# Kernel tuning notes

Hardware: AMD Instinct MI355X
Metric: run time of the kernel (lower is better)

Reference implementation:

```python
import jax, jax.numpy as jnp
import numpy as np

EPS = 1e-5  # torch LayerNorm default
NUM_HEADS = 8


def layernorm(x, g, b):
    m = jnp.mean(x, axis=-1, keepdims=True)
    v = jnp.var(x, axis=-1, keepdims=True)
    return (x - m) * jax.lax.rsqrt(v + EPS) * g + b


def dwconv(x_img, w, b):
    # x_img: [B,C,H,W]; w: [C,1,k,k] depthwise, 'same' padding
    C = x_img.shape[1]
    k = w.shape[-1]
    out = jax.lax.conv_general_dilated(
        x_img, w, (1, 1), [(k // 2, k // 2)] * 2,
        dimension_numbers=('NCHW', 'OIHW', 'NCHW'), feature_group_count=C)
    return out + b[None, :, None, None]


def _forward(x, domain_label, cpe_w, cpe_b, ln1_g, ln1_b, qkv_w, proj_w, proj_b,
             dl_w1, dl_b1, dl_w2, dl_b2, crpe_w3, crpe_b3, crpe_w5, crpe_b5,
             crpe_w7, crpe_b7, ln2_g, ln2_b, fc1_w, fc1_b, fc2_w, fc2_b, H, W, d):
    B, N, C = x.shape
    h = NUM_HEADS
    Ch = C // h
    scale = Ch ** (-0.5)

    # ---- CPE: depthwise 3x3 conv positional encoding with residual ----
    xi = x.transpose(0, 2, 1).reshape(B, C, H, W)
    xi = dwconv(xi, cpe_w, cpe_b) + xi
    x = xi.reshape(B, C, N).transpose(0, 2, 1)

    # ---- domain-indexed LayerNorm 1 (d is a static python int) ----
    cur = layernorm(x, ln1_g[d], ln1_b[d])

    # ---- factorized attention ----
    qkv = (cur @ qkv_w).reshape(B, N, 3, h, Ch).transpose(2, 0, 3, 1, 4)
    q, k, v = qkv[0], qkv[1], qkv[2]          # each [B,h,N,Ch]
    k_sm = jax.nn.softmax(k, axis=2)          # softmax over tokens
    kv = jnp.einsum('bhnk,bhnv->bhkv', k_sm, v)       # [B,h,Ch,Ch]
    factor_att = jnp.einsum('bhnk,bhkv->bhnv', q, kv)  # [B,h,N,Ch]

    # ---- conv relative position encoding (window splits {3:2,5:3,7:3}) ----
    v_img = v.transpose(0, 1, 3, 2).reshape(B, C, H, W)
    g1 = dwconv(v_img[:, :2 * Ch], crpe_w3, crpe_b3)
    g2 = dwconv(v_img[:, 2 * Ch:5 * Ch], crpe_w5, crpe_b5)
    g3 = dwconv(v_img[:, 5 * Ch:], crpe_w7, crpe_b7)
    conv_v = jnp.concatenate([g1, g2, g3], axis=1)        # [B,C,H,W]
    conv_v = conv_v.reshape(B, h, Ch, N).transpose(0, 1, 3, 2)
    crpe = q * conv_v                                      # [B,h,N,Ch]

    factor_att = scale * factor_att + crpe

    # ---- per-domain softmax gating over heads ----
    da = jax.nn.relu(domain_label @ dl_w1 + dl_b1) @ dl_w2 + dl_b2  # [B, h*Ch]
    da = da.reshape(B, h, Ch)[:, :, None, :]                        # [B,h,1,Ch]
    da = jax.nn.softmax(da, axis=1)                                  # over heads
    attn = (da * factor_att).transpose(0, 2, 1, 3).reshape(B, N, C)
    attn = attn @ proj_w + proj_b

    x = x + attn

    # ---- domain-indexed LayerNorm 2 + MLP ----
    cur = layernorm(x, ln2_g[d], ln2_b[d])
    cur = jax.nn.gelu(cur @ fc1_w + fc1_b, approximate=False) @ fc2_w + fc2_b
    return x + cur


def setup_inputs() -> dict:
    key = jax.random.key(0)
    ks = iter(jax.random.split(key, 32))
    B, H, W, C, h, nd = 8, 56, 56, 256, 8, 4
    N = H * W
    Ch = C // h
    hid = C // 2   # domain MLP hidden = max(dim//r,4), r=2
    mh = 4 * C     # mlp_ratio=4
    r = lambda shape, s=0.02: jax.random.normal(next(ks), shape, jnp.float32) * s
    return dict(
        x=jax.random.normal(next(ks), (B, N, C), jnp.float32),
        domain_label=jax.nn.one_hot(
            jax.random.randint(next(ks), (B,), 0, nd), nd, dtype=jnp.float32),
        cpe_w=r((C, 1, 3, 3)), cpe_b=jnp.zeros((C,), jnp.float32),
        ln1_g=jnp.ones((nd, C), jnp.float32), ln1_b=jnp.zeros((nd, C), jnp.float32),
        qkv_w=r((C, 3 * C)),
        proj_w=r((C, C)), proj_b=jnp.zeros((C,), jnp.float32),
        dl_w1=r((nd, hid)), dl_b1=jnp.zeros((hid,), jnp.float32),
        dl_w2=r((hid, C)), dl_b2=jnp.zeros((C,), jnp.float32),
        crpe_w3=r((2 * Ch, 1, 3, 3)), crpe_b3=jnp.zeros((2 * Ch,), jnp.float32),
        crpe_w5=r((3 * Ch, 1, 5, 5)), crpe_b5=jnp.zeros((3 * Ch,), jnp.float32),
        crpe_w7=r((3 * Ch, 1, 7, 7)), crpe_b7=jnp.zeros((3 * Ch,), jnp.float32),
        ln2_g=jnp.ones((nd, C), jnp.float32), ln2_b=jnp.zeros((nd, C), jnp.float32),
        fc1_w=r((C, mh)), fc1_b=jnp.zeros((mh,), jnp.float32),
        fc2_w=r((mh, C)), fc2_b=jnp.zeros((C,), jnp.float32),
        H=H, W=W, d=0,
    )


def reference(x, domain_label, cpe_w, cpe_b, ln1_g, ln1_b, qkv_w, proj_w, proj_b,
              dl_w1, dl_b1, dl_w2, dl_b2, crpe_w3, crpe_b3, crpe_w5, crpe_b5,
              crpe_w7, crpe_b7, ln2_g, ln2_b, fc1_w, fc1_b, fc2_w, fc2_b, H, W, d):
    return _forward(x, domain_label, cpe_w, cpe_b, ln1_g, ln1_b, qkv_w, proj_w,
                    proj_b, dl_w1, dl_b1, dl_w2, dl_b2, crpe_w3, crpe_b3, crpe_w5,
                    crpe_b5, crpe_w7, crpe_b7, ln2_g, ln2_b, fc1_w, fc1_b, fc2_w,
                    fc2_b, H, W, d)
```

## Files before the change

### kernel.cpp

```cpp
#include <hip/hip_runtime.h>
#include <hip/hip_bf16.h>
#include <math.h>

#define BB 8
#define HH 56
#define WW 56
#define NN (HH*WW)
#define CC 256
#define NH 8
#define NT (BB*NN)
#define HID 128
#define MH 1024
#define SCALE 0.17677669529663687f

typedef __attribute__((ext_vector_type(8))) short bf16x8;
typedef __attribute__((ext_vector_type(4))) float f32x4;

__device__ __forceinline__ ushort f2bf(float f) {
    __hip_bfloat16 h = __float2bfloat16(f);
    return *(ushort*)&h;
}
__device__ __forceinline__ uint pk2(float lo, float hi) {
    return ((uint)f2bf(hi) << 16) | (uint)f2bf(lo);
}
__device__ __forceinline__ float unlo(uint u) { return __uint_as_float(u << 16); }
__device__ __forceinline__ float unhi(uint u) { return __uint_as_float(u & 0xFFFF0000u); }

__device__ __forceinline__ void gload16(const void* g, void* s) {
    __builtin_amdgcn_global_load_lds(
        (const __attribute__((address_space(1))) void*)g,
        (__attribute__((address_space(3))) void*)s, 16, 0, 0);
}

__global__ __launch_bounds__(256) void wtrans_kernel(
    const float* __restrict__ w, ushort* __restrict__ wt, int K, int N)
{
    __shared__ float tile[32][33];
    const int t = threadIdx.x;
    const int col = t & 31, rw = t >> 5;
    const int k0 = blockIdx.y * 32, n0 = blockIdx.x * 32;
    #pragma unroll
    for (int i = rw; i < 32; i += 8)
        tile[i][col] = w[(size_t)(k0 + i) * N + n0 + col];
    __syncthreads();
    #pragma unroll
    for (int i = rw; i < 32; i += 8)
        wt[(size_t)(n0 + i) * K + k0 + col] = f2bf(tile[col][i]);
}

__global__ __launch_bounds__(256) void wpack_kernel(
    const float* __restrict__ w3, const float* __restrict__ b3,
    const float* __restrict__ w5, const float* __restrict__ b5,
    const float* __restrict__ w7, const float* __restrict__ b7,
    uint* __restrict__ wt, float* __restrict__ bt)
{
    const int qq = blockIdx.x;
    const int KSQ = (qq == 0) ? 3 : (qq == 1) ? 5 : 7;
    for (int idx = threadIdx.x; idx < 49 * 32; idx += 256) {
        int tap = idx >> 5, p = idx & 31;
        int cA = qq * 64 + 2 * p;
        float lo = 0.f, hi = 0.f;
        if (tap < KSQ * KSQ) {
            int dy = tap / KSQ, dx = tap - dy * KSQ;
            const float* wb; int kslo;
            if (cA < 64)       { wb = w3 + cA * 9;          kslo = 3; }
            else if (cA < 160) { wb = w5 + (cA - 64) * 25;  kslo = 5; }
            else               { wb = w7 + (cA - 160) * 49; kslo = 7; }
            int offp = KSQ / 2 - kslo / 2;
            int sy = dy - offp, sx = dx - offp;
            if (sy >= 0 && sy < kslo && sx >= 0 && sx < kslo) {
                lo = wb[sy * kslo + sx];
                hi = wb[kslo * kslo + sy * kslo + sx];
            }
        }
        wt[(qq * 49 + tap) * 32 + p] = pk2(lo, hi);
    }
    if (threadIdx.x < 32) {
        int p = threadIdx.x, cA = qq * 64 + 2 * p;
        float blo, bhi;
        if (cA < 64)       { blo = b3[cA];       bhi = b3[cA + 1]; }
        else if (cA < 160) { blo = b5[cA - 64];  bhi = b5[cA - 63]; }
        else               { blo = b7[cA - 160]; bhi = b7[cA - 159]; }
        bt[(qq * 32 + p) * 2]     = blo;
        bt[(qq * 32 + p) * 2 + 1] = bhi;
    }
}

__global__ __launch_bounds__(256) void cpack_kernel(
    const float* __restrict__ w, const float* __restrict__ bias,
    uint* __restrict__ wt, float* __restrict__ bt)
{
    const int qq = blockIdx.x;
    for (int idx = threadIdx.x; idx < 9 * 32; idx += 256) {
        int tap = idx >> 5, p = idx & 31;
        int cA = qq * 64 + 2 * p;
        wt[(qq * 9 + tap) * 32 + p] = pk2(w[cA * 9 + tap], w[(cA + 1) * 9 + tap]);
    }
    if (threadIdx.x < 32) {
        int p = threadIdx.x, cA = qq * 64 + 2 * p;
        bt[(qq * 32 + p) * 2]     = bias[cA];
        bt[(qq * 32 + p) * 2 + 1] = bias[cA + 1];
    }
}

__global__ __launch_bounds__(256) void cpe_kernel(
    const float* __restrict__ x, const uint* __restrict__ wtab,
    const float* __restrict__ btab, float* __restrict__ out)
{
    __shared__ uint vt[4 * 34 * 32];
    const int qq = blockIdx.x >> 1, hx = blockIdx.x & 1;
    const int y0 = blockIdx.y * 2, b = blockIdx.z;
    const int x0 = hx * 28;
    const int t = threadIdx.x;
    const int c0 = qq * 64;
    const int p = t & 31;

    uint wpk[9];
    #pragma unroll
    for (int i = 0; i < 9; ++i) wpk[i] = wtab[(qq * 9 + i) * 32 + p];
    const float2 bb = *(const float2*)(btab + (qq * 32 + p) * 2);

    for (int pos = t >> 5; pos < 4 * 34; pos += 8) {
        int row = pos / 34, col = pos - row * 34;
        int gy = y0 + row - 1, gx = x0 + col - 3;
        float2 v = {0.f, 0.f};
        if ((unsigned)gy < 56u && (unsigned)gx < 56u)
            v = *(const float2*)(x + ((size_t)b * NN + gy * 56 + gx) * CC + c0 + 2 * p);
        vt[pos * 32 + p] = pk2(v.x, v.y);
    }
    __syncthreads();

    const int rseg = t >> 5;
    const int r = rseg >> 2, sg = rseg & 3;
    float accA[7], accB[7];
    #pragma unroll
    for (int k = 0; k < 7; ++k) { accA[k] = bb.x; accB[k] = bb.y; }

    #pragma unroll
    for (int dy = 0; dy < 3; ++dy) {
        const int rowbase = (r + dy) * 34 * 32;
        float fA[9], fB[9];
        #pragma unroll
        for (int u = 0; u < 9; ++u) {
            uint vv = vt[rowbase + (sg * 7 + 2 + u) * 32 + p];
            fA[u] = unlo(vv); fB[u] = unhi(vv);
        }
        #pragma unroll
        for (int dx = 0; dx < 3; ++dx) {
            uint wv = wpk[dy * 3 + dx];
            float wl = unlo(wv), wh = unhi(wv);
            #pragma unroll
            for (int k = 0; k < 7; ++k) {
                accA[k] = fmaf(fA[dx + k], wl, accA[k]);
                accB[k] = fmaf(fB[dx + k], wh, accB[k]);
            }
        }
    }

    const int cA = c0 + 2 * p;
    const int ytok = y0 + r;
    #pragma unroll
    for (int k = 0; k < 7; ++k) {
        size_t tok = (size_t)b * NN + ytok * 56 + x0 + sg * 7 + k;
        float2 res = *(const float2*)(x + tok * CC + cA);
        float2 o = { accA[k] + res.x, accB[k] + res.y };
        *(float2*)(out + tok * CC + cA) = o;
    }
}

__global__ __launch_bounds__(256) void ln_kernel(
    const float* __restrict__ src, const float* __restrict__ g_all,
    const float* __restrict__ b_all, const int* __restrict__ dptr,
    ushort* __restrict__ dst)
{
    const int wid = threadIdx.x >> 6, lane = threadIdx.x & 63;
    const int row = blockIdx.x * 4 + wid;
    const int d = *dptr;
    const float* g = g_all + d * CC;
    const float* be = b_all + d * CC;
    const float* p = src + (size_t)row * CC;
    float4 v = *(const float4*)(p + lane * 4);
    float s = v.x + v.y + v.z + v.w;
    float sq = v.x*v.x + v.y*v.y + v.z*v.z + v.w*v.w;
    #pragma unroll
    for (int off = 1; off < 64; off <<= 1) {
        s  += __shfl_xor(s, off);
        sq += __shfl_xor(sq, off);
    }
    const float mean = s * (1.f / CC);
    const float var = sq * (1.f / CC) - mean * mean;
    const float rs = rsqrtf(var + 1e-5f);
    float4 g4 = *(const float4*)(g + lane * 4);
    float4 b4 = *(const float4*)(be + lane * 4);
    ushort4 o4;
    o4.x = f2bf((v.x - mean) * rs * g4.x + b4.x);
    o4.y = f2bf((v.y - mean) * rs * g4.y + b4.y);
    o4.z = f2bf((v.z - mean) * rs * g4.z + b4.z);
    o4.w = f2bf((v.w - mean) * rs * g4.w + b4.w);
    *(ushort4*)(dst + (size_t)row * CC + lane * 4) = o4;
}

template<int EPI>
__global__ __launch_bounds__(256) void gemm_mfma(
    const ushort* __restrict__ A, const ushort* __restrict__ Bt,
    const float* __restrict__ bias, const float* __restrict__ res,
    void* __restrict__ Cv, int M, int N, int K)
{
    __shared__ __align__(16) ushort Als[128 * 32];
    __shared__ __align__(16) ushort Bls[128 * 32];
    const int t = threadIdx.x;
    const int bm = blockIdx.y, bn = blockIdx.x;
    const int brow = bm * 128, bcol = bn * 128;
    const int lane = t & 63, w = t >> 6;
    const int wr = w >> 1, wc = w & 1;
    const int lrow = lane & 15, lko = (lane >> 4) * 8;

    const ushort* gA0 = A + (size_t)(brow + (t >> 2)) * K + (t & 3) * 8;
    const ushort* gA1 = gA0 + (size_t)64 * K;
    const ushort* gB0 = Bt + (size_t)(bcol + (t >> 2)) * K + (t & 3) * 8;
    const ushort* gB1 = gB0 + (size_t)64 * K;
    ushort* lA0 = &Als[t * 8];  ushort* lA1 = &Als[64 * 32 + t * 8];
    ushort* lB0 = &Bls[t * 8];  ushort* lB1 = &Bls[64 * 32 + t * 8];

    f32x4 acc[4][4] = {};

    for (int kt = 0; kt < K; kt += 32) {
        gload16(gA0 + kt, lA0);
        gload16(gA1 + kt, lA1);
        gload16(gB0 + kt, lB0);
        gload16(gB1 + kt, lB1);
        __syncthreads();
        bf16x8 af[4], bfr[4];
        #pragma unroll
        for (int i = 0; i < 4; ++i)
            af[i] = *(const bf16x8*)&Als[(wr * 64 + i * 16 + lrow) * 32 + lko];
        #pragma unroll
        for (int j = 0; j < 4; ++j)
            bfr[j] = *(const bf16x8*)&Bls[(wc * 64 + j * 16 + lrow) * 32 + lko];
        #pragma unroll
        for (int i = 0; i < 4; ++i)
            #pragma unroll
            for (int j = 0; j < 4; ++j)
                acc[i][j] = __builtin_amdgcn_mfma_f32_16x16x32_bf16(
                    af[i], bfr[j], acc[i][j], 0, 0, 0);
        __syncthreads();
    }

    float* Cf = (float*)Cv;
    ushort* Ch = (ushort*)Cv;
    #pragma unroll
    for (int j = 0; j < 4; ++j) {
        const int col = bcol + wc * 64 + j * 16 + lrow;
        const float bv = (EPI >= 2) ? bias[col] : 0.f;
        #pragma unroll
        for (int i = 0; i < 4; ++i) {
            const int row0 = brow + wr * 64 + i * 16 + (lane >> 4) * 4;
            #pragma unroll
            for (int r = 0; r < 4; ++r) {
                float v = acc[i][j][r] + bv;
                size_t off = (size_t)(row0 + r) * N + col;
                if (EPI == 2) {
                    v = 0.5f * v * (1.f + erff(v * 0.70710678118654752f));
                    Ch[off] = f2bf(v);
                } else if (EPI == 3) {
                    Cf[off] = v + res[off];
                } else {
                    Cf[off] = v;
                }
            }
        }
    }
}

__global__ __launch_bounds__(256) void kmax1_kernel(
    const float* __restrict__ qkv, float* __restrict__ pmax)
{
    const int chunk = blockIdx.x, b = blockIdx.y, c = threadIdx.x;
    const float* kb = qkv + (size_t)(b * NN + chunk * 98) * 768 + 256 + c;
    float m = -3.4e38f;
    for (int i = 0; i < 98; ++i) m = fmaxf(m, kb[(size_t)i * 768]);
    pmax[(b * 32 + chunk) * CC + c] = m;
}

__global__ __launch_bounds__(256) void kmax2_kernel(
    const float* __restrict__ pmax, float* __restrict__ cmax)
{
    const int b = blockIdx.x, c = threadIdx.x;
    float m = -3.4e38f;
    #pragma unroll
    for (int i = 0; i < 32; ++i) m = fmaxf(m, pmax[(b * 32 + i) * CC + c]);
    cmax[b * CC + c] = m;
}

__global__ __launch_bounds__(256) void kvacc_kernel(
    const float* __restrict__ qkv, const float* __restrict__ cmax,
    float* __restrict__ partial, float* __restrict__ psum)
{
    const int chunk = blockIdx.x, h = blockIdx.y, b = blockIdx.z;
    const int t = threadIdx.x;
    const int ck = t & 31, g = t >> 5;
    const int n0 = chunk * 196;
    const float* kb = qkv + (size_t)(b * NN + n0) * 768 + 256 + h * 32 + ck;
    const float* vb = qkv + (size_t)(b * NN + n0) * 768 + 512 + h * 32 + g * 4;
    const float cm = cmax[b * CC + h * 32 + ck];
    float a0 = 0.f, a1 = 0.f, a2 = 0.f, a3 = 0.f, s = 0.f;
    for (int i = 0; i < 196; ++i) {
        float e = __expf(kb[(size_t)i * 768] - cm);
        float4 v4 = *(const float4*)(vb + (size_t)i * 768);
        a0 += e * v4.x; a1 += e * v4.y; a2 += e * v4.z; a3 += e * v4.w;
        s += e;
    }
    float4 o = {a0, a1, a2, a3};
    *(float4*)(partial + ((((size_t)chunk * 8 + b) * 8 + h) * 32 + ck) * 32 + g * 4) = o;
    if (g == 0) psum[((chunk * 8 + b) * 8 + h) * 32 + ck] = s;
}

__global__ __launch_bounds__(256) void kvnorm_kernel(
    const float* __restrict__ partial, const float* __restrict__ psum,
    float* __restrict__ kv)
{
    const int idx = blockIdx.x * 256 + threadIdx.x;
    const int ckidx = idx >> 5;
    float sum = 0.f, cs = 0.f;
    #pragma unroll
    for (int ch = 0; ch < 16; ++ch) {
        sum += partial[(size_t)ch * 65536 + idx];
        cs  += psum[ch * 2048 + ckidx];
    }
    kv[idx] = sum / cs;
}

__global__ __launch_bounds__(256) void fa_kernel(
    float* __restrict__ qkv, const float* __restrict__ kvb)
{
    const int mt = blockIdx.x, h = blockIdx.y, b = blockIdx.z;
    const int t = threadIdx.x;
    const int lane = t & 63, wv = t >> 6;
    const int row0 = mt * 448 + wv * 112;
    const int lr = lane & 15, lk = (lane >> 4) * 8;

    bf16x8 bfr[2];
    #pragma unroll
    for (int jj = 0; jj < 2; ++jj)
        #pragma unroll
        for (int e = 0; e < 8; ++e)
            bfr[jj][e] = (short)f2bf(kvb[((size_t)(b * 8 + h) * 32 + lk + e) * 32 + jj * 16 + lr]);

    #pragma unroll
    for (int i = 0; i < 7; ++i) {
        size_t tok = (size_t)b * NN + row0 + i * 16 + lr;
        const float* qp = qkv + tok * 768 + h * 32 + lk;
        float4 qa = *(const float4*)qp;
        float4 qb2 = *(const float4*)(qp + 4);
        bf16x8 af;
        af[0] = (short)f2bf(qa.x);  af[1] = (short)f2bf(qa.y);
        af[2] = (short)f2bf(qa.z);  af[3] = (short)f2bf(qa.w);
        af[4] = (short)f2bf(qb2.x); af[5] = (short)f2bf(qb2.y);
        af[6] = (short)f2bf(qb2.z); af[7] = (short)f2bf(qb2.w);
        f32x4 a0 = {0.f, 0.f, 0.f, 0.f}, a1 = {0.f, 0.f, 0.f, 0.f};
        a0 = __builtin_amdgcn_mfma_f32_16x16x32_bf16(af, bfr[0], a0, 0, 0, 0);
        a1 = __builtin_amdgcn_mfma_f32_16x16x32_bf16(af, bfr[1], a1, 0, 0, 0);
        #pragma unroll
        for (int r = 0; r < 4; ++r) {
            size_t trow = (size_t)b * NN + row0 + i * 16 + (lane >> 4) * 4 + r;
            qkv[trow * 768 + 256 + h * 32 + lr]      = a0[r];
            qkv[trow * 768 + 256 + h * 32 + 16 + lr] = a1[r];
        }
    }
}

__global__ __launch_bounds__(256) void da_kernel(
    const float* __restrict__ dl, const float* __restrict__ w1,
    const float* __restrict__ b1, const float* __restrict__ w2,
    const float* __restrict__ b2, float* __restrict__ da)
{
    const int b = blockIdx.x, t = threadIdx.x;
    __shared__ float r[HID];
    __shared__ float raw[CC];
    if (t < HID) {
        float s = b1[t];
        #pragma unroll
        for (int k = 0; k < 4; ++k) s += dl[b * 4 + k] * w1[k * HID + t];
        r[t] = fmaxf(s, 0.f);
    }
    __syncthreads();
    float s = b2[t];
    for (int j = 0; j < HID; ++j) s += r[j] * w2[j * CC + t];
    raw[t] = s;
    __syncthreads();
    const int ch = t & 31;
    float m = -3.4e38f;
    #pragma unroll
    for (int hh = 0; hh < NH; ++hh) m = fmaxf(m, raw[hh * 32 + ch]);
    float ssum = 0.f;
    #pragma unroll
    for (int hh = 0; hh < NH; ++hh) ssum += __expf(raw[hh * 32 + ch] - m);
    da[b * CC + t] = __expf(raw[t] - m) / ssum;
}

template<int KS>
__device__ __forceinline__ void comb_body(
    uint* vt, int qq,
    const float* __restrict__ qkv, const float* __restrict__ da,
    const uint* __restrict__ wtab, const float* __restrict__ btab,
    ushort* __restrict__ out)
{
    constexpr int R = KS / 2;
    constexpr int TR = KS + 1;
    constexpr int WCOLS = 7 + 2 * R;
    const int hx = blockIdx.x & 1;
    const int y0 = blockIdx.y * 2, b = blockIdx.z;
    const int x0 = hx * 28;
    const int t = threadIdx.x;
    const int c0 = qq * 64;
    const int p = t & 31;

    uint wpk[KS * KS];
    #pragma unroll
    for (int i = 0; i < KS * KS; ++i) wpk[i] = wtab[(qq * 49 + i) * 32 + p];
    const float2 bb = *(const float2*)(btab + (qq * 32 + p) * 2);

    for (int pos = t >> 5; pos < TR * 34; pos += 8) {
        int row = pos / 34, col = pos - row * 34;
        int gy = y0 + row - R, gx = x0 + col - 3;
        float2 v = {0.f, 0.f};
        if ((unsigned)gy < 56u && (unsigned)gx < 56u)
            v = *(const float2*)(qkv + ((size_t)b * NN + gy * 56 + gx) * 768 + 512 + c0 + 2 * p);
        vt[pos * 32 + p] = pk2(v.x, v.y);
    }
    __syncthreads();

    const int rseg = t >> 5;
    const int r = rseg >> 2, sg = rseg & 3;
    float accA[7], accB[7];
    #pragma unroll
    for (int k = 0; k < 7; ++k) { accA[k] = bb.x; accB[k] = bb.y; }

    #pragma unroll
    for (int dy = 0; dy < KS; ++dy) {
        const int rowbase = (r + dy) * 34 * 32;
        float fA[WCOLS], fB[WCOLS];
        #pragma unroll
        for (int u = 0; u < WCOLS; ++u) {
            uint vv = vt[rowbase + (sg * 7 + 3 - R + u) * 32 + p];
            fA[u] = unlo(vv); fB[u] = unhi(vv);
        }
        #pragma unroll
        for (int dx = 0; dx < KS; ++dx) {
            uint wv = wpk[dy * KS + dx];
            float wl = unlo(wv), wh = unhi(wv);
            #pragma unroll
            for (int k = 0; k < 7; ++k) {
                accA[k] = fmaf(fA[dx + k], wl, accA[k]);
                accB[k] = fmaf(fB[dx + k], wh, accB[k]);
            }
        }
    }

    const int cA = c0 + 2 * p;
    const float2 da2 = *(const float2*)(da + b * CC + cA);
    const int ytok = y0 + r;
    #pragma unroll
    for (int k = 0; k < 7; ++k) {
        size_t tok = (size_t)b * NN + ytok * 56 + x0 + sg * 7 + k;
        float2 q2 = *(const float2*)(qkv + tok * 768 + cA);
        float2 fa2 = *(const float2*)(qkv + tok * 768 + 256 + cA);
        ushort2 o = { f2bf(da2.x * (SCALE * fa2.x + q2.x * accA[k])),
                      f2bf(da2.y * (SCALE * fa2.y + q2.y * accB[k])) };
        *(ushort2*)(out + tok * CC + cA) = o;
    }
}

__global__ __launch_bounds__(256) void combine_kernel(
    const float* __restrict__ qkv, const float* __restrict__ da,
    const uint* __restrict__ wtab, const float* __restrict__ btab,
    ushort* __restrict__ out)
{
    __shared__ uint vt[8 * 34 * 32];
    switch (blockIdx.x >> 1) {
    case 0:  comb_body<3>(vt, 0, qkv, da, wtab, btab, out); break;
    case 1:  comb_body<5>(vt, 1, qkv, da, wtab, btab, out); break;
    case 2:  comb_body<7>(vt, 2, qkv, da, wtab, btab, out); break;
    default: comb_body<7>(vt, 3, qkv, da, wtab, btab, out); break;
    }
}

extern "C" void kernel_launch(void* const* d_in, const int* in_sizes, int n_in,
                              void* d_out, int out_size, void* d_ws, size_t ws_size,
                              hipStream_t stream)
{
    const float* x       = (const float*)d_in[0];
    const float* dlab    = (const float*)d_in[1];
    const float* cpe_w   = (const float*)d_in[2];
    const float* cpe_b   = (const float*)d_in[3];
    const float* ln1_g   = (const float*)d_in[4];
    const float* ln1_b   = (const float*)d_in[5];
    const float* qkv_w   = (const float*)d_in[6];
    const float* proj_w  = (const float*)d_in[7];
    const float* proj_b  = (const float*)d_in[8];
    const float* dl_w1   = (const float*)d_in[9];
    const float* dl_b1   = (const float*)d_in[10];
    const float* dl_w2   = (const float*)d_in[11];
    const float* dl_b2   = (const float*)d_in[12];
    const float* crpe_w3 = (const float*)d_in[13];
    const float* crpe_b3 = (const float*)d_in[14];
    const float* crpe_w5 = (const float*)d_in[15];
    const float* crpe_b5 = (const float*)d_in[16];
    const float* crpe_w7 = (const float*)d_in[17];
    const float* crpe_b7 = (const float*)d_in[18];
    const float* ln2_g   = (const float*)d_in[19];
    const float* ln2_b   = (const float*)d_in[20];
    const float* fc1_w   = (const float*)d_in[21];
    const float* fc1_b   = (const float*)d_in[22];
    const float* fc2_w   = (const float*)d_in[23];
    const float* fc2_b   = (const float*)d_in[24];
    const int*   dptr    = (const int*)d_in[27];

    float* out = (float*)d_out;
    char* W = (char*)d_ws;
    size_t off = 0;
    float* x1 = (float*)(W + off);          off += (size_t)NT * CC * 4;
    float* qkv = (float*)(W + off);
    ushort* hidden = (ushort*)qkv;
    off += (size_t)NT * 768 * 4;
    ushort* actbf = (ushort*)(W + off);     off += (size_t)NT * CC * 2;
    float* partial = (float*)actbf;
    float* psum = partial + (size_t)16 * 65536;
    float* kvb = (float*)(W + off);         off += (size_t)65536 * 4;
    float* dab = (float*)(W + off);         off += (size_t)BB * CC * 4;
    float* pmax = (float*)(W + off);        off += (size_t)BB * 32 * CC * 4;
    float* cmax = (float*)(W + off);        off += (size_t)BB * CC * 4;
    ushort* wq  = (ushort*)(W + off);       off += (size_t)768 * 256 * 2;
    ushort* wp  = (ushort*)(W + off);       off += (size_t)256 * 256 * 2;
    ushort* w1t = (ushort*)(W + off);       off += (size_t)1024 * 256 * 2;
    ushort* w2t = (ushort*)(W + off);       off += (size_t)256 * 1024 * 2;
    uint* wcomb = (uint*)(W + off);         off += (size_t)4 * 49 * 32 * 4;
    float* bcomb = (float*)(W + off);       off += (size_t)4 * 32 * 2 * 4;
    uint* wcpe = (uint*)(W + off);          off += (size_t)4 * 9 * 32 * 4;
    float* bcpe = (float*)(W + off);        off += (size_t)4 * 32 * 2 * 4;

    hipLaunchKernelGGL(wpack_kernel, dim3(4), dim3(256), 0, stream,
                       crpe_w3, crpe_b3, crpe_w5, crpe_b5, crpe_w7, crpe_b7, wcomb, bcomb);
    hipLaunchKernelGGL(cpack_kernel, dim3(4), dim3(256), 0, stream, cpe_w, cpe_b, wcpe, bcpe);
    hipLaunchKernelGGL(wtrans_kernel, dim3(768 / 32, 256 / 32), dim3(256), 0, stream, qkv_w, wq, 256, 768);
    hipLaunchKernelGGL(wtrans_kernel, dim3(256 / 32, 256 / 32), dim3(256), 0, stream, proj_w, wp, 256, 256);
    hipLaunchKernelGGL(wtrans_kernel, dim3(1024 / 32, 256 / 32), dim3(256), 0, stream, fc1_w, w1t, 256, 1024);
    hipLaunchKernelGGL(wtrans_kernel, dim3(256 / 32, 1024 / 32), dim3(256), 0, stream, fc2_w, w2t, 1024, 256);
    hipLaunchKernelGGL(cpe_kernel, dim3(8, 28, 8), dim3(256), 0, stream, x, wcpe, bcpe, x1);
    hipLaunchKernelGGL(da_kernel, dim3(BB), dim3(256), 0, stream,
                       dlab, dl_w1, dl_b1, dl_w2, dl_b2, dab);
    hipLaunchKernelGGL(ln_kernel, dim3(NT / 4), dim3(256), 0, stream,
                       x1, ln1_g, ln1_b, dptr, actbf);
    hipLaunchKernelGGL(gemm_mfma<0>, dim3(768 / 128, NT / 128), dim3(256), 0, stream,
                       actbf, wq, nullptr, nullptr, (void*)qkv, NT, 768, 256);
    hipLaunchKernelGGL(kmax1_kernel, dim3(32, 8), dim3(256), 0, stream, qkv, pmax);
    hipLaunchKernelGGL(kmax2_kernel, dim3(8), dim3(256), 0, stream, pmax, cmax);
    hipLaunchKernelGGL(kvacc_kernel, dim3(16, 8, 8), dim3(256), 0, stream,
                       qkv, cmax, partial, psum);
    hipLaunchKernelGGL(kvnorm_kernel, dim3(256), dim3(256), 0, stream,
                       partial, psum, kvb);
    hipLaunchKernelGGL(fa_kernel, dim3(7, 8, 8), dim3(256), 0, stream, qkv, kvb);
    hipLaunchKernelGGL(combine_kernel, dim3(8, 28, 8), dim3(256), 0, stream,
                       qkv, dab, wcomb, bcomb, actbf);
    hipLaunchKernelGGL(gemm_mfma<3>, dim3(256 / 128, NT / 128), dim3(256), 0, stream,
                       actbf, wp, proj_b, x1, (void*)out, NT, 256, 256);
    hipLaunchKernelGGL(ln_kernel, dim3(NT / 4), dim3(256), 0, stream,
                       out, ln2_g, ln2_b, dptr, actbf);
    hipLaunchKernelGGL(gemm_mfma<2>, dim3(1024 / 128, NT / 128), dim3(256), 0, stream,
                       actbf, w1t, fc1_b, nullptr, (void*)hidden, NT, 1024, 256);
    hipLaunchKernelGGL(gemm_mfma<3>, dim3(256 / 128, NT / 128), dim3(256), 0, stream,
                       hidden, w2t, fc2_b, out, (void*)out, NT, 256, 1024);
}
```

Baseline: 426.2 us.

## Store qkv in bf16, vectorize GEMM epilogue via permuted weights, XCD-aware block mapping

The qkv intermediate is now stored as bf16 instead of fp32, which halves the traffic of the QKV GEMM store and of the attention kernels that read it (kmax, kvacc, fa, combine). Weight columns are permuted within each 64-column group so that every lane owns four contiguous output columns. This lets the GEMM epilogue write float4 or ushort4 values instead of scalar stores. GEMM launches become 1D with a remap that places neighbouring tiles on the same XCD for L2 locality. The cost is reduced precision for q, k, v and the factor-attention output held in bf16.

```diff
diff --git a/kernel.cpp b/kernel.cpp
--- a/kernel.cpp
+++ b/kernel.cpp
@@ -20,6 +20,9 @@
     __hip_bfloat16 h = __float2bfloat16(f);
     return *(ushort*)&h;
 }
+__device__ __forceinline__ float bf2f(ushort u) {
+    union { unsigned int i; float f; } x; x.i = ((unsigned int)u) << 16; return x.f;
+}
 __device__ __forceinline__ uint pk2(float lo, float hi) {
     return ((uint)f2bf(hi) << 16) | (uint)f2bf(lo);
 }
@@ -44,8 +47,12 @@
         tile[i][col] = w[(size_t)(k0 + i) * N + n0 + col];
     __syncthreads();
     #pragma unroll
-    for (int i = rw; i < 32; i += 8)
-        wt[(size_t)(n0 + i) * K + k0 + col] = f2bf(tile[col][i]);
+    for (int i = rw; i < 32; i += 8) {
+        int n = n0 + i;
+        int nl = n & 63;
+        int np = (n & ~63) | ((nl & 3) * 16 + (nl >> 2));
+        wt[(size_t)np * K + k0 + col] = f2bf(tile[col][i]);
+    }
 }
 
 __global__ __launch_bounds__(256) void wpack_kernel(
@@ -204,12 +211,16 @@
 __global__ __launch_bounds__(256) void gemm_mfma(
     const ushort* __restrict__ A, const ushort* __restrict__ Bt,
     const float* __restrict__ bias, const float* __restrict__ res,
-    void* __restrict__ Cv, int M, int N, int K)
+    void* __restrict__ Cv, int M, int N, int K, int nbn, int nwg)
 {
     __shared__ __align__(16) ushort Als[128 * 32];
     __shared__ __align__(16) ushort Bls[128 * 32];
     const int t = threadIdx.x;
-    const int bm = blockIdx.y, bn = blockIdx.x;
+    const int lin = blockIdx.x;
+    const int q8 = nwg >> 3, r8 = nwg & 7;
+    const int xcd = lin & 7, i8 = lin >> 3;
+    const int wgid = (xcd < r8 ? xcd * (q8 + 1) : r8 * (q8 + 1) + (xcd - r8) * q8) + i8;
+    const int bm = wgid / nbn, bn = wgid - bm * nbn;
     const int brow = bm * 128, bcol = bn * 128;
     const int lane = t & 63, w = t >> 6;
     const int wr = w >> 1, wc = w & 1;
@@ -248,37 +259,46 @@
 
     float* Cf = (float*)Cv;
     ushort* Ch = (ushort*)Cv;
-    #pragma unroll
-    for (int j = 0; j < 4; ++j) {
-        const int col = bcol + wc * 64 + j * 16 + lrow;
-        const float bv = (EPI >= 2) ? bias[col] : 0.f;
-        #pragma unroll
-        for (int i = 0; i < 4; ++i) {
-            const int row0 = brow + wr * 64 + i * 16 + (lane >> 4) * 4;
+    const int col0 = bcol + wc * 64 + 4 * lrow;
+    float bias4[4] = {0.f, 0.f, 0.f, 0.f};
+    if (EPI >= 2) {
+        float4 bv = *(const float4*)(bias + col0);
+        bias4[0] = bv.x; bias4[1] = bv.y; bias4[2] = bv.z; bias4[3] = bv.w;
+    }
+    #pragma unroll
+    for (int i = 0; i < 4; ++i) {
+        #pragma unroll
+        for (int r = 0; r < 4; ++r) {
+            const int row = brow + wr * 64 + i * 16 + (lane >> 4) * 4 + r;
+            size_t off = (size_t)row * N + col0;
+            float o[4];
             #pragma unroll
-            for (int r = 0; r < 4; ++r) {
-                float v = acc[i][j][r] + bv;
-                size_t off = (size_t)(row0 + r) * N + col;
-                if (EPI == 2) {
-                    v = 0.5f * v * (1.f + erff(v * 0.70710678118654752f));
-                    Ch[off] = f2bf(v);
-                } else if (EPI == 3) {
-                    Cf[off] = v + res[off];
-                } else {
-                    Cf[off] = v;
-                }
+            for (int j = 0; j < 4; ++j) o[j] = acc[i][j][r] + bias4[j];
+            if (EPI == 2) {
+                #pragma unroll
+                for (int j = 0; j < 4; ++j)
+                    o[j] = 0.5f * o[j] * (1.f + erff(o[j] * 0.70710678118654752f));
+                ushort4 st = { f2bf(o[0]), f2bf(o[1]), f2bf(o[2]), f2bf(o[3]) };
+                *(ushort4*)(Ch + off) = st;
+            } else if (EPI == 1) {
+                ushort4 st = { f2bf(o[0]), f2bf(o[1]), f2bf(o[2]), f2bf(o[3]) };
+                *(ushort4*)(Ch + off) = st;
+            } else {
+                float4 rv = *(const float4*)(res + off);
+                float4 st = { o[0] + rv.x, o[1] + rv.y, o[2] + rv.z, o[3] + rv.w };
+                *(float4*)(Cf + off) = st;
             }
         }
     }
 }
 
 __global__ __launch_bounds__(256) void kmax1_kernel(
-    const float* __restrict__ qkv, float* __restrict__ pmax)
+    const ushort* __restrict__ qkv, float* __restrict__ pmax)
 {
     const int chunk = blockIdx.x, b = blockIdx.y, c = threadIdx.x;
-    const float* kb = qkv + (size_t)(b * NN + chunk * 98) * 768 + 256 + c;
+    const ushort* kb = qkv + (size_t)(b * NN + chunk * 98) * 768 + 256 + c;
     float m = -3.4e38f;
-    for (int i = 0; i < 98; ++i) m = fmaxf(m, kb[(size_t)i * 768]);
+    for (int i = 0; i < 98; ++i) m = fmaxf(m, bf2f(kb[(size_t)i * 768]));
     pmax[(b * 32 + chunk) * CC + c] = m;
 }
 
@@ -293,21 +313,22 @@
 }
 
 __global__ __launch_bounds__(256) void kvacc_kernel(
-    const float* __restrict__ qkv, const float* __restrict__ cmax,
+    const ushort* __restrict__ qkv, const float* __restrict__ cmax,
     float* __restrict__ partial, float* __restrict__ psum)
 {
     const int chunk = blockIdx.x, h = blockIdx.y, b = blockIdx.z;
     const int t = threadIdx.x;
     const int ck = t & 31, g = t >> 5;
     const int n0 = chunk * 196;
-    const float* kb = qkv + (size_t)(b * NN + n0) * 768 + 256 + h * 32 + ck;
-    const float* vb = qkv + (size_t)(b * NN + n0) * 768 + 512 + h * 32 + g * 4;
+    const ushort* kb = qkv + (size_t)(b * NN + n0) * 768 + 256 + h * 32 + ck;
+    const ushort* vb = qkv + (size_t)(b * NN + n0) * 768 + 512 + h * 32 + g * 4;
     const float cm = cmax[b * CC + h * 32 + ck];
     float a0 = 0.f, a1 = 0.f, a2 = 0.f, a3 = 0.f, s = 0.f;
     for (int i = 0; i < 196; ++i) {
-        float e = __expf(kb[(size_t)i * 768] - cm);
-        float4 v4 = *(const float4*)(vb + (size_t)i * 768);
-        a0 += e * v4.x; a1 += e * v4.y; a2 += e * v4.z; a3 += e * v4.w;
+        float e = __expf(bf2f(kb[(size_t)i * 768]) - cm);
+        ushort4 v4 = *(const ushort4*)(vb + (size_t)i * 768);
+        a0 += e * bf2f(v4.x); a1 += e * bf2f(v4.y);
+        a2 += e * bf2f(v4.z); a3 += e * bf2f(v4.w);
         s += e;
     }
     float4 o = {a0, a1, a2, a3};
@@ -331,7 +352,7 @@
 }
 
 __global__ __launch_bounds__(256) void fa_kernel(
-    float* __restrict__ qkv, const float* __restrict__ kvb)
+    ushort* __restrict__ qkv, const float* __restrict__ kvb)
 {
     const int mt = blockIdx.x, h = blockIdx.y, b = blockIdx.z;
     const int t = threadIdx.x;
@@ -344,27 +365,19 @@
     for (int jj = 0; jj < 2; ++jj)
         #pragma unroll
         for (int e = 0; e < 8; ++e)
-            bfr[jj][e] = (short)f2bf(kvb[((size_t)(b * 8 + h) * 32 + lk + e) * 32 + jj * 16 + lr]);
+            bfr[jj][e] = (short)f2bf(kvb[((size_t)(b * 8 + h) * 32 + lk + e) * 32 + 2 * lr + jj]);
 
     #pragma unroll
     for (int i = 0; i < 7; ++i) {
         size_t tok = (size_t)b * NN + row0 + i * 16 + lr;
-        const float* qp = qkv + tok * 768 + h * 32 + lk;
-        float4 qa = *(const float4*)qp;
-        float4 qb2 = *(const float4*)(qp + 4);
-        bf16x8 af;
-        af[0] = (short)f2bf(qa.x);  af[1] = (short)f2bf(qa.y);
-        af[2] = (short)f2bf(qa.z);  af[3] = (short)f2bf(qa.w);
-        af[4] = (short)f2bf(qb2.x); af[5] = (short)f2bf(qb2.y);
-        af[6] = (short)f2bf(qb2.z); af[7] = (short)f2bf(qb2.w);
+        bf16x8 af = *(const bf16x8*)(qkv + tok * 768 + h * 32 + lk);
         f32x4 a0 = {0.f, 0.f, 0.f, 0.f}, a1 = {0.f, 0.f, 0.f, 0.f};
         a0 = __builtin_amdgcn_mfma_f32_16x16x32_bf16(af, bfr[0], a0, 0, 0, 0);
         a1 = __builtin_amdgcn_mfma_f32_16x16x32_bf16(af, bfr[1], a1, 0, 0, 0);
         #pragma unroll
         for (int r = 0; r < 4; ++r) {
             size_t trow = (size_t)b * NN + row0 + i * 16 + (lane >> 4) * 4 + r;
-            qkv[trow * 768 + 256 + h * 32 + lr]      = a0[r];
-            qkv[trow * 768 + 256 + h * 32 + 16 + lr] = a1[r];
+            *(uint*)(qkv + trow * 768 + 256 + h * 32 + 2 * lr) = pk2(a0[r], a1[r]);
         }
     }
 }
@@ -401,7 +414,7 @@
 template<int KS>
 __device__ __forceinline__ void comb_body(
     uint* vt, int qq,
-    const float* __restrict__ qkv, const float* __restrict__ da,
+    const ushort* __restrict__ qkv, const float* __restrict__ da,
     const uint* __restrict__ wtab, const float* __restrict__ btab,
     ushort* __restrict__ out)
 {
@@ -423,10 +436,10 @@
     for (int pos = t >> 5; pos < TR * 34; pos += 8) {
         int row = pos / 34, col = pos - row * 34;
         int gy = y0 + row - R, gx = x0 + col - 3;
-        float2 v = {0.f, 0.f};
+        uint v = 0;
         if ((unsigned)gy < 56u && (unsigned)gx < 56u)
-            v = *(const float2*)(qkv + ((size_t)b * NN + gy * 56 + gx) * 768 + 512 + c0 + 2 * p);
-        vt[pos * 32 + p] = pk2(v.x, v.y);
+            v = *(const uint*)(qkv + ((size_t)b * NN + gy * 56 + gx) * 768 + 512 + c0 + 2 * p);
+        vt[pos * 32 + p] = v;
     }
     __syncthreads();
 
@@ -463,16 +476,16 @@
     #pragma unroll
     for (int k = 0; k < 7; ++k) {
         size_t tok = (size_t)b * NN + ytok * 56 + x0 + sg * 7 + k;
-        float2 q2 = *(const float2*)(qkv + tok * 768 + cA);
-        float2 fa2 = *(const float2*)(qkv + tok * 768 + 256 + cA);
-        ushort2 o = { f2bf(da2.x * (SCALE * fa2.x + q2.x * accA[k])),
-                      f2bf(da2.y * (SCALE * fa2.y + q2.y * accB[k])) };
+        uint qw = *(const uint*)(qkv + tok * 768 + cA);
+        uint fw = *(const uint*)(qkv + tok * 768 + 256 + cA);
+        ushort2 o = { f2bf(da2.x * (SCALE * unlo(fw) + unlo(qw) * accA[k])),
+                      f2bf(da2.y * (SCALE * unhi(fw) + unhi(qw) * accB[k])) };
         *(ushort2*)(out + tok * CC + cA) = o;
     }
 }
 
 __global__ __launch_bounds__(256) void combine_kernel(
-    const float* __restrict__ qkv, const float* __restrict__ da,
+    const ushort* __restrict__ qkv, const float* __restrict__ da,
     const uint* __restrict__ wtab, const float* __restrict__ btab,
     ushort* __restrict__ out)
 {
@@ -520,9 +533,8 @@
     char* W = (char*)d_ws;
     size_t off = 0;
     float* x1 = (float*)(W + off);          off += (size_t)NT * CC * 4;
-    float* qkv = (float*)(W + off);
-    ushort* hidden = (ushort*)qkv;
-    off += (size_t)NT * 768 * 4;
+    ushort* qkvb = (ushort*)(W + off);
+    ushort* hidden = (ushort*)(W + off);    off += (size_t)NT * MH * 2;
     ushort* actbf = (ushort*)(W + off);     off += (size_t)NT * CC * 2;
     float* partial = (float*)actbf;
     float* psum = partial + (size_t)16 * 65536;
@@ -551,23 +563,23 @@
                        dlab, dl_w1, dl_b1, dl_w2, dl_b2, dab);
     hipLaunchKernelGGL(ln_kernel, dim3(NT / 4), dim3(256), 0, stream,
                        x1, ln1_g, ln1_b, dptr, actbf);
-    hipLaunchKernelGGL(gemm_mfma<0>, dim3(768 / 128, NT / 128), dim3(256), 0, stream,
-                       actbf, wq, nullptr, nullptr, (void*)qkv, NT, 768, 256);
-    hipLaunchKernelGGL(kmax1_kernel, dim3(32, 8), dim3(256), 0, stream, qkv, pmax);
+    hipLaunchKernelGGL(gemm_mfma<1>, dim3(196 * 6), dim3(256), 0, stream,
+                       actbf, wq, nullptr, nullptr, (void*)qkvb, NT, 768, 256, 6, 196 * 6);
+    hipLaunchKernelGGL(kmax1_kernel, dim3(32, 8), dim3(256), 0, stream, qkvb, pmax);
     hipLaunchKernelGGL(kmax2_kernel, dim3(8), dim3(256), 0, stream, pmax, cmax);
     hipLaunchKernelGGL(kvacc_kernel, dim3(16, 8, 8), dim3(256), 0, stream,
-                       qkv, cmax, partial, psum);
+                       qkvb, cmax, partial, psum);
     hipLaunchKernelGGL(kvnorm_kernel, dim3(256), dim3(256), 0, stream,
                        partial, psum, kvb);
-    hipLaunchKernelGGL(fa_kernel, dim3(7, 8, 8), dim3(256), 0, stream, qkv, kvb);
+    hipLaunchKernelGGL(fa_kernel, dim3(7, 8, 8), dim3(256), 0, stream, qkvb, kvb);
     hipLaunchKernelGGL(combine_kernel, dim3(8, 28, 8), dim3(256), 0, stream,
-                       qkv, dab, wcomb, bcomb, actbf);
-    hipLaunchKernelGGL(gemm_mfma<3>, dim3(256 / 128, NT / 128), dim3(256), 0, stream,
-                       actbf, wp, proj_b, x1, (void*)out, NT, 256, 256);
+                       qkvb, dab, wcomb, bcomb, actbf);
+    hipLaunchKernelGGL(gemm_mfma<3>, dim3(196 * 2), dim3(256), 0, stream,
+                       actbf, wp, proj_b, x1, (void*)out, NT, 256, 256, 2, 196 * 2);
     hipLaunchKernelGGL(ln_kernel, dim3(NT / 4), dim3(256), 0, stream,
                        out, ln2_g, ln2_b, dptr, actbf);
-    hipLaunchKernelGGL(gemm_mfma<2>, dim3(1024 / 128, NT / 128), dim3(256), 0, stream,
-                       actbf, w1t, fc1_b, nullptr, (void*)hidden, NT, 1024, 256);
-    hipLaunchKernelGGL(gemm_mfma<3>, dim3(256 / 128, NT / 128), dim3(256), 0, stream,
-                       hidden, w2t, fc2_b, out, (void*)out, NT, 256, 1024);
-}
+    hipLaunchKernelGGL(gemm_mfma<2>, dim3(196 * 8), dim3(256), 0, stream,
+                       actbf, w1t, fc1_b, nullptr, (void*)hidden, NT, 1024, 256, 8, 196 * 8);
+    hipLaunchKernelGGL(gemm_mfma<3>, dim3(196 * 2), dim3(256), 0, stream,
+                       hidden, w2t, fc2_b, out, (void*)out, NT, 256, 1024, 2, 196 * 2);
+}
```

Measured after the change: 396.6 us. 1.07x faster.
